# Performance work log

Hardware: AMD Instinct MI355X
Metric: run time of the kernel (lower is better)

## Reference

```python
import jax, jax.numpy as jnp
import numpy as np

NEG_SLOPE = 0.2
MASK_FILL = -1e9


def setup_inputs() -> dict:
    key = jax.random.key(0)
    k1, k2, k3, k4 = jax.random.split(key, 4)
    B, N, IN_DIM = 4, 2048, 256
    H, D = 8, 64  # n_heads, hidden_dim (out_dim)
    nodes = jax.random.normal(k1, (B, N, IN_DIM), dtype=jnp.float32)
    edges = jax.random.randint(k2, (B, N, N), 0, 2, dtype=jnp.int32)
    # Xavier-uniform-ish init for params
    pw_lim = float(np.sqrt(6.0 / (IN_DIM + H * D)))
    proj_weights = jax.random.uniform(k3, (IN_DIM, H * D), dtype=jnp.float32,
                                      minval=-pw_lim, maxval=pw_lim)
    aw_lim = float(np.sqrt(6.0 / (H + 2 * D)))
    attn_weights = jax.random.uniform(k4, (H, 2 * D), dtype=jnp.float32,
                                      minval=-aw_lim, maxval=aw_lim)
    return {"nodes": nodes, "edges": edges,
            "proj_weights": proj_weights, "attn_weights": attn_weights}


def reference(nodes, edges, proj_weights, attn_weights):
    B, N, _ = nodes.shape
    H, twoD = attn_weights.shape
    D = twoD // 2
    # Projection: [B,N,in] @ [in,H*D] -> [B,H,N,D]
    mapped = jnp.matmul(nodes, proj_weights).reshape(B, N, H, D).transpose(0, 2, 1, 3)
    # The left@diag(a)@right^T trick is exactly a_l.h_i + a_r.h_j:
    a_l = attn_weights[:, :D]   # [H,D]
    a_r = attn_weights[:, D:]   # [H,D]
    el = jnp.einsum('bhnd,hd->bhn', mapped, a_l)  # score contribution of source i
    er = jnp.einsum('bhnd,hd->bhn', mapped, a_r)  # score contribution of target j
    scores = jax.nn.leaky_relu(el[:, :, :, None] + er[:, :, None, :],
                               negative_slope=NEG_SLOPE)  # [B,H,N,N]
    scores = jnp.where(edges[:, None, :, :] == 0, MASK_FILL, scores)
    attn = jax.nn.softmax(scores, axis=-1)  # dropout p=0 -> identity
    out = jnp.einsum('bhij,bhjd->bhid', attn, mapped)  # [B,H,N,D]
    out = out.transpose(0, 2, 1, 3).reshape(B, N, H * D)  # is_concat=True
    return jax.nn.sigmoid(out)
```

## Files before the change

### kernel.cpp

```cpp
#include <hip/hip_runtime.h>
#include <hip/hip_fp16.h>
#include <math.h>

#define NEG 0.2f
#define LOG2E 1.4426950408889634f

typedef float f32x4 __attribute__((ext_vector_type(4)));
typedef _Float16 half8 __attribute__((ext_vector_type(8)));
typedef _Float16 h2v __attribute__((ext_vector_type(2)));

extern "C" __device__ _Float16 __ocml_exp2_f16(_Float16);

__device__ inline uint cvt2(float a, float b) {
  union {
    decltype(__builtin_amdgcn_cvt_pkrtz(0.f, 0.f)) v;
    uint u;
  } x;
  x.v = __builtin_amdgcn_cvt_pkrtz(a, b);
  return x.u;
}

__device__ inline h2v u2h(uint u) {
  union {
    uint u;
    h2v v;
  } x;
  x.u = u;
  return x.v;
}

__device__ inline uint h2u(h2v v) {
  union {
    uint u;
    h2v v;
  } x;
  x.v = v;
  return x.u;
}

__global__ __launch_bounds__(256) void prep_kernel(const float* __restrict__ W,
                                                   ushort* __restrict__ wf,
                                                   uint* __restrict__ ermx) {
  const int bx = blockIdx.x;
  const int t = threadIdx.x;
  if (bx == 32) {
    if (t < 32) ermx[t] = 0u;
    return;
  }
  const int h = bx >> 2, ct = bx & 3;
#pragma unroll
  for (int s = 0; s < 2; ++s) {
    int slot = t + s * 256;
    int l = slot & 63, kk = slot >> 6;
    int col = h * 64 + ct * 16 + (l & 15);
    int k0 = kk * 32 + (l >> 4) * 8;
    uint outv[4];
#pragma unroll
    for (int c = 0; c < 4; ++c) {
      float x0 = W[(size_t)(k0 + 2 * c) * 512 + col];
      float x1 = W[(size_t)(k0 + 2 * c + 1) * 512 + col];
      outv[c] = cvt2(x0, x1);
    }
    *(uint4*)&wf[(((size_t)((h * 4 + ct) * 8 + kk)) * 64 + l) * 8] = *(uint4*)outv;
  }
}

__global__ __launch_bounds__(256, 4) void pack_proj(
    const int* __restrict__ e, unsigned long long* __restrict__ epk64,
    const float* __restrict__ A, const ushort* __restrict__ wf,
    const float* __restrict__ aw, ushort* __restrict__ mt,
    float* __restrict__ el, float* __restrict__ er, uint* __restrict__ ermx) {
  __shared__ ushort ct_lds[64][72];
  const int bx = blockIdx.x;
  const int t = threadIdx.x;
  const int l = t & 63;
  if (bx % 5 != 4) {
    const int pack_id = (bx / 5) * 4 + (bx % 5);
    const int wid = pack_id * 4 + (t >> 6);
    const size_t base = (size_t)wid * 1024;
#pragma unroll
    for (int it = 0; it < 4; ++it) {
      const size_t off = base + it * 256;
      unsigned long long b0 = __ballot(e[off + l] != 0);
      unsigned long long b1 = __ballot(e[off + 64 + l] != 0);
      unsigned long long b2 = __ballot(e[off + 128 + l] != 0);
      unsigned long long b3 = __ballot(e[off + 192 + l] != 0);
      if (l == 0) {
        ulonglong2 p0, p1;
        p0.x = b0;
        p0.y = b1;
        p1.x = b2;
        p1.y = b3;
        *(ulonglong2*)&epk64[off >> 6] = p0;
        *(ulonglong2*)&epk64[(off >> 6) + 2] = p1;
      }
    }
    return;
  }
  const int pid = bx / 5;
  const int wq = t >> 6;
  const int i0 = (pid & 127) * 64;
  const int h = pid >> 7;
  const int b = i0 >> 11, n0 = i0 & 2047, bh = b * 8 + h;
  const int cl = l & 15, hi = l >> 4;
  const float* arow = A + (size_t)(i0 + wq * 16 + cl) * 256 + hi * 8;
  const int4* wfb = (const int4*)wf + (size_t)h * 32 * 64 + l;
  f32x4 acc[4];
#pragma unroll
  for (int ct = 0; ct < 4; ++ct) acc[ct] = (f32x4){0.f, 0.f, 0.f, 0.f};
#pragma unroll
  for (int kk = 0; kk < 8; ++kk) {
    float4 a0 = *(const float4*)(arow + kk * 32);
    float4 a1 = *(const float4*)(arow + kk * 32 + 4);
    union {
      uint u[4];
      half8 v;
    } af;
    af.u[0] = cvt2(a0.x, a0.y);
    af.u[1] = cvt2(a0.z, a0.w);
    af.u[2] = cvt2(a1.x, a1.y);
    af.u[3] = cvt2(a1.z, a1.w);
#pragma unroll
    for (int ct = 0; ct < 4; ++ct) {
      union {
        int4 i;
        half8 v;
      } bf;
      bf.i = wfb[((size_t)ct * 8 + kk) * 64];
      acc[ct] = __builtin_amdgcn_mfma_f32_16x16x32_f16(af.v, bf.v, acc[ct], 0, 0, 0);
    }
  }
  float alc[4], arc[4];
#pragma unroll
  for (int ct = 0; ct < 4; ++ct) {
    alc[ct] = aw[h * 128 + ct * 16 + cl];
    arc[ct] = aw[h * 128 + 64 + ct * 16 + cl];
  }
  float ermax_loc = -1e30f;
#pragma unroll
  for (int reg = 0; reg < 4; ++reg) {
    float pl = acc[0][reg] * alc[0] + acc[1][reg] * alc[1] + acc[2][reg] * alc[2] +
               acc[3][reg] * alc[3];
    float pr = acc[0][reg] * arc[0] + acc[1][reg] * arc[1] + acc[2][reg] * arc[2] +
               acc[3][reg] * arc[3];
#pragma unroll
    for (int s = 1; s < 16; s <<= 1) {
      pl += __shfl_xor(pl, s);
      pr += __shfl_xor(pr, s);
    }
    if (cl == 0) {
      int n = n0 + wq * 16 + hi * 4 + reg;
      el[(size_t)bh * 2048 + n] = pl;
      er[(size_t)bh * 2048 + n] = pr;
    }
    ermax_loc = fmaxf(ermax_loc, pr);
  }
  ermax_loc = fmaxf(ermax_loc, __shfl_xor(ermax_loc, 16));
  ermax_loc = fmaxf(ermax_loc, __shfl_xor(ermax_loc, 32));
  if (l == 0) {
    uint bits = __float_as_uint(ermax_loc);
    uint key = (bits & 0x80000000u) ? ~bits : (bits | 0x80000000u);
    atomicMax(&ermx[bh], key);
  }
#pragma unroll
  for (int ct = 0; ct < 4; ++ct) {
    ushort4 us;
    us.x = __half_as_ushort(__float2half(acc[ct][0]));
    us.y = __half_as_ushort(__float2half(acc[ct][1]));
    us.z = __half_as_ushort(__float2half(acc[ct][2]));
    us.w = __half_as_ushort(__float2half(acc[ct][3]));
    *(ushort4*)&ct_lds[ct * 16 + cl][wq * 16 + hi * 4] = us;
  }
  __syncthreads();
  {
    const int f = t >> 5, s = t & 31;
    const int g = f >> 2, nt = f & 3;
    const int r = nt * 16 + (s & 15);
    const int cm = g * 32 + (s >> 4) * 8;
    int4 v0 = *(const int4*)&ct_lds[r][cm];
    int4 v1 = *(const int4*)&ct_lds[r][cm + 16];
    const size_t base = ((size_t)bh * 32 + (n0 >> 6)) * 4096 + f * 512;
    *(int4*)&mt[base + s * 8] = v0;
    *(int4*)&mt[base + (s + 32) * 8] = v1;
  }
}

__global__ __launch_bounds__(512, 8) void gat_attn(const ushort* __restrict__ mt,
                                                   const uint* __restrict__ epk,
                                                   const float* __restrict__ el,
                                                   const float* __restrict__ er,
                                                   const uint* __restrict__ ermx,
                                                   float* __restrict__ out) {
  __shared__ __align__(16) char smem[36864];
  int4* vt4 = (int4*)smem;
  uint* ersh = (uint*)(smem + 32768);
  const int t = threadIdx.x;
  const int l = t & 63;
  const int hf = t >> 8;
  const int th = t & 255;
  const int wq = (t >> 6) & 3;
  const int r16 = l & 15, hi = l >> 4;
  const int sh8 = hi * 8;
  const int i0 = blockIdx.x * 64;
  const int h = blockIdx.y, b = blockIdx.z;
  const int bh = b * 8 + h;
  if (t < 256) {
    float4 e0 = *(const float4*)&er[(size_t)bh * 2048 + t * 8];
    float4 e1 = *(const float4*)&er[(size_t)bh * 2048 + t * 8 + 4];
    uint4 pk;
    pk.x = cvt2(e0.x, e0.y);
    pk.y = cvt2(e0.z, e0.w);
    pk.z = cvt2(e1.x, e1.y);
    pk.w = cvt2(e1.z, e1.w);
    *(uint4*)&ersh[t * 4] = pk;
  }
  const int irow = i0 + wq * 16 + r16;
  const float el_r = el[(size_t)bh * 2048 + irow];
  const uint ky = ermx[bh];
  const float emx = __uint_as_float((ky & 0x80000000u) ? (ky ^ 0x80000000u) : ~ky);
  const float s0 = el_r + emx;
  const float m_r = fmaxf(s0, NEG * s0);
  const float m2 = m_r * LOG2E;
  const float cAf = __builtin_fmaf(el_r, LOG2E, -m2);
  const float cBf = __builtin_fmaf(el_r, NEG * LOG2E, -m2);
  const h2v cA2 = {(_Float16)cAf, (_Float16)cAf};
  const h2v cB2 = {(_Float16)cBf, (_Float16)cBf};
  const h2v l2e2 = {(_Float16)LOG2E, (_Float16)LOG2E};
  const h2v nl2e2 = {(_Float16)(NEG * LOG2E), (_Float16)(NEG * LOG2E)};
  const uint* erow = epk + (size_t)(b * 2048 + irow) * 64;
  f32x4 acc[4];
  f32x4 accL = {0.f, 0.f, 0.f, 0.f};
#pragma unroll
  for (int nt = 0; nt < 4; ++nt) acc[nt] = (f32x4){0.f, 0.f, 0.f, 0.f};
  half8 ones;
#pragma unroll
  for (int c = 0; c < 8; ++c) ones[c] = (_Float16)1.f;

  const int jtg0 = hf * 16;
  const int4* srcbase = (const int4*)mt + ((size_t)bh * 32 + jtg0) * 512 + wq * 128 + l;
  unsigned long long ew = *(const unsigned long long*)(erow + jtg0 * 2);
  {
    int4 p0 = srcbase[0];
    int4 p1 = srcbase[64];
    int4* d = vt4 + hf * 512 + wq * 128 + l;
    d[0] = p0;
    d[64] = p1;
  }
  __syncthreads();
  int cur = 0;
  for (int jt = 0; jt < 16; ++jt) {
    int4 nx0, nx1;
    unsigned long long ewn;
    if (jt < 15) {
      const int4* s = srcbase + (size_t)(jt + 1) * 512;
      nx0 = s[0];
      nx1 = s[64];
      ewn = *(const unsigned long long*)(erow + (jtg0 + jt + 1) * 2);
    }
    const uint wsh0 = ((uint)ew) >> sh8;
    const uint wsh1 = ((uint)(ew >> 32)) >> sh8;
    const int j0 = (jtg0 + jt) * 64;
    half8 af[2];
#pragma unroll
    for (int g = 0; g < 2; ++g) {
      uint4 uv = *(const uint4*)&ersh[(j0 >> 1) + g * 16 + hi * 4];
      uint uvw[4] = {uv.x, uv.y, uv.z, uv.w};
      const uint wg = g ? wsh1 : wsh0;
      union {
        uint u[4];
        half8 v8;
      } fr;
#pragma unroll
      for (int q = 0; q < 4; ++q) {
        h2v u2 = u2h(uvw[q]);
#if __has_builtin(__builtin_elementwise_fma)
        h2v a2 = __builtin_elementwise_fma(u2, l2e2, cA2);
        h2v b2 = __builtin_elementwise_fma(u2, nl2e2, cB2);
#else
        h2v a2 = u2 * l2e2 + cA2;
        h2v b2 = u2 * nl2e2 + cB2;
#endif
        h2v t2 = __builtin_elementwise_max(a2, b2);
        h2v p2;
        p2[0] = __ocml_exp2_f16(t2[0]);
        p2[1] = __ocml_exp2_f16(t2[1]);
        uint pu = h2u(p2);
        uint mlo = (uint)(((int)(wg << (31 - 2 * q))) >> 31);
        uint mhi = (uint)(((int)(wg << (30 - 2 * q))) >> 31);
        uint mask2 = (mlo & 0x0000FFFFu) | (mhi & 0xFFFF0000u);
        fr.u[q] = pu & mask2;
      }
      af[g] = fr.v8;
    }
    const half8* fb = (const half8*)(vt4 + cur * 1024 + hf * 512);
    __builtin_amdgcn_s_setprio(1);
#pragma unroll
    for (int g = 0; g < 2; ++g) {
      accL = __builtin_amdgcn_mfma_f32_16x16x32_f16(af[g], ones, accL, 0, 0, 0);
#pragma unroll
      for (int nt = 0; nt < 4; ++nt) {
        half8 bfr = fb[(g * 4 + nt) * 64 + l];
        acc[nt] = __builtin_amdgcn_mfma_f32_16x16x32_f16(af[g], bfr, acc[nt], 0, 0, 0);
      }
    }
    __builtin_amdgcn_s_setprio(0);
    if (jt < 15) {
      int4* d = vt4 + (cur ^ 1) * 1024 + hf * 512 + wq * 128 + l;
      d[0] = nx0;
      d[64] = nx1;
      ew = ewn;
    }
    __syncthreads();
    cur ^= 1;
  }
  float* red = (float*)smem;
  if (hf == 1) {
    float* dst = red + th * 21;
#pragma unroll
    for (int nt = 0; nt < 4; ++nt)
#pragma unroll
      for (int k = 0; k < 4; ++k) dst[nt * 4 + k] = acc[nt][k];
#pragma unroll
    for (int k = 0; k < 4; ++k) dst[16 + k] = accL[k];
  }
  __syncthreads();
  if (hf == 0) {
    const float* src = red + th * 21;
#pragma unroll
    for (int reg = 0; reg < 4; ++reg) {
      float Lrow = accL[reg] + src[16 + reg];
      float invL = 1.f / Lrow;
      int orow = i0 + wq * 16 + hi * 4 + reg;
#pragma unroll
      for (int nt = 0; nt < 4; ++nt) {
        float o = (acc[nt][reg] + src[nt * 4 + reg]) * invL;
        float sig = 1.f / (1.f + __expf(-o));
        out[(size_t)(b * 2048 + orow) * 512 + h * 64 + nt * 16 + r16] = sig;
      }
    }
  }
}

extern "C" void kernel_launch(void* const* d_in, const int* in_sizes, int n_in,
                              void* d_out, int out_size, void* d_ws, size_t ws_size,
                              hipStream_t stream) {
  const float* nodes = (const float*)d_in[0];
  const int* edges = (const int*)d_in[1];
  const float* pw = (const float*)d_in[2];
  const float* aw = (const float*)d_in[3];
  float* out = (float*)d_out;

  ushort* mt = (ushort*)d_ws;
  float* el = (float*)((char*)d_ws + 8388608);
  float* er = (float*)((char*)d_ws + 8650752);
  uint* ermx = (uint*)((char*)d_ws + 8912896);
  uint* epk = (uint*)((char*)d_ws + 8913024);
  ushort* wf = (ushort*)((char*)d_ws + 11010176);

  prep_kernel<<<33, 256, 0, stream>>>(pw, wf, ermx);
  pack_proj<<<5120, 256, 0, stream>>>(edges, (unsigned long long*)epk, nodes, wf, aw,
                                      mt, el, er, ermx);
  gat_attn<<<dim3(32, 8, 4), 512, 0, stream>>>(mt, epk, el, er, ermx, out);
}
```

Measured before the change: 91.33 us.

## Factor softmax exponent into precomputed exp terms and restructure edge bitmask packing

Uses exp(a+b) = exp(a)*exp(b) to precompute per-column exp2 factors for both leaky-relu branches in shared memory and per-row scale factors. The per-element exp2 in the inner loop becomes two fp16 multiplies and a max. Edge packing now loads int4 vectors with an interleaved bit layout, and half of the packing is moved into the prep kernel so it runs ahead of the projection. The risks are fp16 overflow or underflow of the exp factors, since er is unbounded, and more complex bit extraction.

```diff
diff --git a/kernel.cpp b/kernel.cpp
--- a/kernel.cpp
+++ b/kernel.cpp
@@ -8,8 +8,13 @@
 typedef float f32x4 __attribute__((ext_vector_type(4)));
 typedef _Float16 half8 __attribute__((ext_vector_type(8)));
 typedef _Float16 h2v __attribute__((ext_vector_type(2)));
-
-extern "C" __device__ _Float16 __ocml_exp2_f16(_Float16);
+typedef short s16x2 __attribute__((ext_vector_type(2)));
+
+#if __has_builtin(__builtin_amdgcn_exp2f)
+#define EXP2F(x) __builtin_amdgcn_exp2f(x)
+#else
+#define EXP2F(x) exp2f(x)
+#endif
 
 __device__ inline uint cvt2(float a, float b) {
   union {
@@ -38,34 +43,67 @@
   return x.u;
 }
 
-__global__ __launch_bounds__(256) void prep_kernel(const float* __restrict__ W,
-                                                   ushort* __restrict__ wf,
-                                                   uint* __restrict__ ermx) {
+__device__ inline uint sgn16(uint t) {
+  union {
+    uint u;
+    s16x2 v;
+  } x;
+  x.u = t;
+  x.v = x.v >> 15;
+  return x.u;
+}
+
+__global__ __launch_bounds__(256, 4) void prep_pack(
+    const float* __restrict__ W, ushort* __restrict__ wf, uint* __restrict__ ermx,
+    const int* __restrict__ e, unsigned long long* __restrict__ epk64) {
   const int bx = blockIdx.x;
   const int t = threadIdx.x;
-  if (bx == 32) {
-    if (t < 32) ermx[t] = 0u;
+  const int l = t & 63;
+  if (bx < 33) {
+    if (bx == 32) {
+      if (t < 32) ermx[t] = 0u;
+      return;
+    }
+    const int h = bx >> 2, ct = bx & 3;
+#pragma unroll
+    for (int s = 0; s < 2; ++s) {
+      int slot = t + s * 256;
+      int ll = slot & 63, kk = slot >> 6;
+      int col = h * 64 + ct * 16 + (ll & 15);
+      int k0 = kk * 32 + (ll >> 4) * 8;
+      uint outv[4];
+#pragma unroll
+      for (int c = 0; c < 4; ++c) {
+        float x0 = W[(size_t)(k0 + 2 * c) * 512 + col];
+        float x1 = W[(size_t)(k0 + 2 * c + 1) * 512 + col];
+        outv[c] = cvt2(x0, x1);
+      }
+      *(uint4*)&wf[(((size_t)((h * 4 + ct) * 8 + kk)) * 64 + ll) * 8] = *(uint4*)outv;
+    }
     return;
   }
-  const int h = bx >> 2, ct = bx & 3;
-#pragma unroll
-  for (int s = 0; s < 2; ++s) {
-    int slot = t + s * 256;
-    int l = slot & 63, kk = slot >> 6;
-    int col = h * 64 + ct * 16 + (l & 15);
-    int k0 = kk * 32 + (l >> 4) * 8;
-    uint outv[4];
-#pragma unroll
-    for (int c = 0; c < 4; ++c) {
-      float x0 = W[(size_t)(k0 + 2 * c) * 512 + col];
-      float x1 = W[(size_t)(k0 + 2 * c + 1) * 512 + col];
-      outv[c] = cvt2(x0, x1);
-    }
-    *(uint4*)&wf[(((size_t)((h * 4 + ct) * 8 + kk)) * 64 + l) * 8] = *(uint4*)outv;
-  }
-}
-
-__global__ __launch_bounds__(256, 4) void pack_proj(
+  const size_t g0 = (size_t)(bx - 33) * 16 + (t >> 6) * 4;
+#pragma unroll
+  for (int it = 0; it < 4; ++it) {
+    const size_t gi = g0 + it;
+    int4 v = *(const int4*)(e + gi * 256 + l * 4);
+    unsigned long long b0 = __ballot(v.x != 0);
+    unsigned long long b1 = __ballot(v.y != 0);
+    unsigned long long b2 = __ballot(v.z != 0);
+    unsigned long long b3 = __ballot(v.w != 0);
+    if (l == 0) {
+      ulonglong2 q0, q1;
+      q0.x = b0;
+      q0.y = b1;
+      q1.x = b2;
+      q1.y = b3;
+      *(ulonglong2*)&epk64[gi * 4] = q0;
+      *(ulonglong2*)&epk64[gi * 4 + 2] = q1;
+    }
+  }
+}
+
+__global__ __launch_bounds__(256, 4) void pack2_proj(
     const int* __restrict__ e, unsigned long long* __restrict__ epk64,
     const float* __restrict__ A, const ushort* __restrict__ wf,
     const float* __restrict__ aw, ushort* __restrict__ mt,
@@ -74,30 +112,30 @@
   const int bx = blockIdx.x;
   const int t = threadIdx.x;
   const int l = t & 63;
-  if (bx % 5 != 4) {
-    const int pack_id = (bx / 5) * 4 + (bx % 5);
-    const int wid = pack_id * 4 + (t >> 6);
-    const size_t base = (size_t)wid * 1024;
+  if (bx % 3 != 2) {
+    const int pb = (bx / 3) * 2 + (bx % 3);
+    const size_t g0 = 32768 + (size_t)pb * 16 + (t >> 6) * 4;
 #pragma unroll
     for (int it = 0; it < 4; ++it) {
-      const size_t off = base + it * 256;
-      unsigned long long b0 = __ballot(e[off + l] != 0);
-      unsigned long long b1 = __ballot(e[off + 64 + l] != 0);
-      unsigned long long b2 = __ballot(e[off + 128 + l] != 0);
-      unsigned long long b3 = __ballot(e[off + 192 + l] != 0);
+      const size_t gi = g0 + it;
+      int4 v = *(const int4*)(e + gi * 256 + l * 4);
+      unsigned long long b0 = __ballot(v.x != 0);
+      unsigned long long b1 = __ballot(v.y != 0);
+      unsigned long long b2 = __ballot(v.z != 0);
+      unsigned long long b3 = __ballot(v.w != 0);
       if (l == 0) {
-        ulonglong2 p0, p1;
-        p0.x = b0;
-        p0.y = b1;
-        p1.x = b2;
-        p1.y = b3;
-        *(ulonglong2*)&epk64[off >> 6] = p0;
-        *(ulonglong2*)&epk64[(off >> 6) + 2] = p1;
+        ulonglong2 q0, q1;
+        q0.x = b0;
+        q0.y = b1;
+        q1.x = b2;
+        q1.y = b3;
+        *(ulonglong2*)&epk64[gi * 4] = q0;
+        *(ulonglong2*)&epk64[gi * 4 + 2] = q1;
       }
     }
     return;
   }
-  const int pid = bx / 5;
+  const int pid = bx / 3;
   const int wq = t >> 6;
   const int i0 = (pid & 127) * 64;
   const int h = pid >> 7;
@@ -185,49 +223,45 @@
   }
 }
 
-__global__ __launch_bounds__(512, 8) void gat_attn(const ushort* __restrict__ mt,
-                                                   const uint* __restrict__ epk,
-                                                   const float* __restrict__ el,
-                                                   const float* __restrict__ er,
-                                                   const uint* __restrict__ ermx,
-                                                   float* __restrict__ out) {
-  __shared__ __align__(16) char smem[36864];
+__global__ __launch_bounds__(512, 8) void gat_attn(
+    const ushort* __restrict__ mt, const unsigned long long* __restrict__ epk64,
+    const float* __restrict__ el, const float* __restrict__ er,
+    const uint* __restrict__ ermx, float* __restrict__ out) {
+  __shared__ __align__(16) char smem[40960];
   int4* vt4 = (int4*)smem;
-  uint* ersh = (uint*)(smem + 32768);
+  uint* ysh = (uint*)(smem + 32768);
+  uint* vsh = (uint*)(smem + 36864);
   const int t = threadIdx.x;
   const int l = t & 63;
   const int hf = t >> 8;
   const int th = t & 255;
   const int wq = (t >> 6) & 3;
   const int r16 = l & 15, hi = l >> 4;
-  const int sh8 = hi * 8;
   const int i0 = blockIdx.x * 64;
   const int h = blockIdx.y, b = blockIdx.z;
   const int bh = b * 8 + h;
-  if (t < 256) {
-    float4 e0 = *(const float4*)&er[(size_t)bh * 2048 + t * 8];
-    float4 e1 = *(const float4*)&er[(size_t)bh * 2048 + t * 8 + 4];
-    uint4 pk;
-    pk.x = cvt2(e0.x, e0.y);
-    pk.y = cvt2(e0.z, e0.w);
-    pk.z = cvt2(e1.x, e1.y);
-    pk.w = cvt2(e1.z, e1.w);
-    *(uint4*)&ersh[t * 4] = pk;
+  {
+    float4 e0 = *(const float4*)&er[(size_t)bh * 2048 + t * 4];
+    uint2 yp, vp;
+    yp.x = cvt2(EXP2F(e0.x * LOG2E), EXP2F(e0.y * LOG2E));
+    yp.y = cvt2(EXP2F(e0.z * LOG2E), EXP2F(e0.w * LOG2E));
+    vp.x = cvt2(EXP2F(e0.x * (NEG * LOG2E)), EXP2F(e0.y * (NEG * LOG2E)));
+    vp.y = cvt2(EXP2F(e0.z * (NEG * LOG2E)), EXP2F(e0.w * (NEG * LOG2E)));
+    *(uint2*)&ysh[t * 2] = yp;
+    *(uint2*)&vsh[t * 2] = vp;
   }
   const int irow = i0 + wq * 16 + r16;
   const float el_r = el[(size_t)bh * 2048 + irow];
   const uint ky = ermx[bh];
   const float emx = __uint_as_float((ky & 0x80000000u) ? (ky ^ 0x80000000u) : ~ky);
   const float s0 = el_r + emx;
-  const float m_r = fmaxf(s0, NEG * s0);
-  const float m2 = m_r * LOG2E;
-  const float cAf = __builtin_fmaf(el_r, LOG2E, -m2);
-  const float cBf = __builtin_fmaf(el_r, NEG * LOG2E, -m2);
-  const h2v cA2 = {(_Float16)cAf, (_Float16)cAf};
-  const h2v cB2 = {(_Float16)cBf, (_Float16)cBf};
-  const h2v l2e2 = {(_Float16)LOG2E, (_Float16)LOG2E};
-  const h2v nl2e2 = {(_Float16)(NEG * LOG2E), (_Float16)(NEG * LOG2E)};
-  const uint* erow = epk + (size_t)(b * 2048 + irow) * 64;
+  const float m2 = fmaxf(s0, NEG * s0) * LOG2E;
+  const float Xf = EXP2F(__builtin_fmaf(el_r, LOG2E, -m2));
+  const float Uf = EXP2F(__builtin_fmaf(el_r, NEG * LOG2E, -m2));
+  const h2v X2 = u2h(cvt2(Xf, Xf));
+  const h2v U2 = u2h(cvt2(Uf, Uf));
+  const unsigned long long* prow =
+      epk64 + ((size_t)(b * 2048 + irow) * 8 + hf * 4) * 4;
   f32x4 acc[4];
   f32x4 accL = {0.f, 0.f, 0.f, 0.f};
 #pragma unroll
@@ -236,9 +270,7 @@
 #pragma unroll
   for (int c = 0; c < 8; ++c) ones[c] = (_Float16)1.f;
 
-  const int jtg0 = hf * 16;
-  const int4* srcbase = (const int4*)mt + ((size_t)bh * 32 + jtg0) * 512 + wq * 128 + l;
-  unsigned long long ew = *(const unsigned long long*)(erow + jtg0 * 2);
+  const int4* srcbase = (const int4*)mt + ((size_t)bh * 32 + hf * 16) * 512 + wq * 128 + l;
   {
     int4 p0 = srcbase[0];
     int4 p1 = srcbase[64];
@@ -248,70 +280,66 @@
   }
   __syncthreads();
   int cur = 0;
-  for (int jt = 0; jt < 16; ++jt) {
-    int4 nx0, nx1;
-    unsigned long long ewn;
-    if (jt < 15) {
-      const int4* s = srcbase + (size_t)(jt + 1) * 512;
-      nx0 = s[0];
-      nx1 = s[64];
-      ewn = *(const unsigned long long*)(erow + (jtg0 + jt + 1) * 2);
-    }
-    const uint wsh0 = ((uint)ew) >> sh8;
-    const uint wsh1 = ((uint)(ew >> 32)) >> sh8;
-    const int j0 = (jtg0 + jt) * 64;
-    half8 af[2];
-#pragma unroll
-    for (int g = 0; g < 2; ++g) {
-      uint4 uv = *(const uint4*)&ersh[(j0 >> 1) + g * 16 + hi * 4];
-      uint uvw[4] = {uv.x, uv.y, uv.z, uv.w};
-      const uint wg = g ? wsh1 : wsh0;
-      union {
-        uint u[4];
-        half8 v8;
-      } fr;
-#pragma unroll
-      for (int q = 0; q < 4; ++q) {
-        h2v u2 = u2h(uvw[q]);
-#if __has_builtin(__builtin_elementwise_fma)
-        h2v a2 = __builtin_elementwise_fma(u2, l2e2, cA2);
-        h2v b2 = __builtin_elementwise_fma(u2, nl2e2, cB2);
-#else
-        h2v a2 = u2 * l2e2 + cA2;
-        h2v b2 = u2 * nl2e2 + cB2;
-#endif
-        h2v t2 = __builtin_elementwise_max(a2, b2);
-        h2v p2;
-        p2[0] = __ocml_exp2_f16(t2[0]);
-        p2[1] = __ocml_exp2_f16(t2[1]);
-        uint pu = h2u(p2);
-        uint mlo = (uint)(((int)(wg << (31 - 2 * q))) >> 31);
-        uint mhi = (uint)(((int)(wg << (30 - 2 * q))) >> 31);
-        uint mask2 = (mlo & 0x0000FFFFu) | (mhi & 0xFFFF0000u);
-        fr.u[q] = pu & mask2;
-      }
-      af[g] = fr.v8;
-    }
-    const half8* fb = (const half8*)(vt4 + cur * 1024 + hf * 512);
-    __builtin_amdgcn_s_setprio(1);
-#pragma unroll
-    for (int g = 0; g < 2; ++g) {
-      accL = __builtin_amdgcn_mfma_f32_16x16x32_f16(af[g], ones, accL, 0, 0, 0);
-#pragma unroll
-      for (int nt = 0; nt < 4; ++nt) {
-        half8 bfr = fb[(g * 4 + nt) * 64 + l];
-        acc[nt] = __builtin_amdgcn_mfma_f32_16x16x32_f16(af[g], bfr, acc[nt], 0, 0, 0);
-      }
-    }
-    __builtin_amdgcn_s_setprio(0);
-    if (jt < 15) {
-      int4* d = vt4 + (cur ^ 1) * 1024 + hf * 512 + wq * 128 + l;
-      d[0] = nx0;
-      d[64] = nx1;
-      ew = ewn;
-    }
-    __syncthreads();
-    cur ^= 1;
+  int jt = 0;
+  for (int gq = 0; gq < 4; ++gq) {
+    const ulonglong2 pA = *(const ulonglong2*)(prow + gq * 4);
+    const ulonglong2 pB = *(const ulonglong2*)(prow + gq * 4 + 2);
+#pragma unroll
+    for (int q4 = 0; q4 < 4; ++q4, ++jt) {
+      int4 nx0, nx1;
+      if (jt < 15) {
+        const int4* s = srcbase + (size_t)(jt + 1) * 512;
+        nx0 = s[0];
+        nx1 = s[64];
+      }
+      const int Bb = q4 * 16 + hi * 2;
+      half8 af[2];
+#pragma unroll
+      for (int g = 0; g < 2; ++g) {
+        const uint idx = (hf * 16 + jt) * 32 + g * 16 + hi * 4;
+        uint4 y4 = *(const uint4*)&ysh[idx];
+        uint4 v4 = *(const uint4*)&vsh[idx];
+        const int sh = Bb + g * 8;
+        uint w0 = (uint)(pA.x >> sh), w1 = (uint)(pA.y >> sh);
+        uint w2 = (uint)(pB.x >> sh), w3 = (uint)(pB.y >> sh);
+        uint tk0 = ((w0 << 15) & 0x8000u) | (w1 << 31);
+        uint tk1 = ((w2 << 15) & 0x8000u) | (w3 << 31);
+        uint tk2 = ((w0 << 14) & 0x8000u) | ((w1 << 30) & 0x80000000u);
+        uint tk3 = ((w2 << 14) & 0x8000u) | ((w3 << 30) & 0x80000000u);
+        uint yq[4] = {y4.x, y4.y, y4.z, y4.w};
+        uint vq[4] = {v4.x, v4.y, v4.z, v4.w};
+        uint tq[4] = {tk0, tk1, tk2, tk3};
+        union {
+          uint u[4];
+          half8 v8;
+        } fr;
+#pragma unroll
+        for (int q = 0; q < 4; ++q) {
+          h2v P2 = __builtin_elementwise_max(X2 * u2h(yq[q]), U2 * u2h(vq[q]));
+          fr.u[q] = h2u(P2) & sgn16(tq[q]);
+        }
+        af[g] = fr.v8;
+      }
+      const half8* fb = (const half8*)(vt4 + cur * 1024 + hf * 512);
+      __builtin_amdgcn_s_setprio(1);
+#pragma unroll
+      for (int g = 0; g < 2; ++g) {
+        accL = __builtin_amdgcn_mfma_f32_16x16x32_f16(af[g], ones, accL, 0, 0, 0);
+#pragma unroll
+        for (int nt = 0; nt < 4; ++nt) {
+          half8 bfr = fb[(g * 4 + nt) * 64 + l];
+          acc[nt] = __builtin_amdgcn_mfma_f32_16x16x32_f16(af[g], bfr, acc[nt], 0, 0, 0);
+        }
+      }
+      __builtin_amdgcn_s_setprio(0);
+      if (jt < 15) {
+        int4* d = vt4 + (cur ^ 1) * 1024 + hf * 512 + wq * 128 + l;
+        d[0] = nx0;
+        d[64] = nx1;
+      }
+      __syncthreads();
+      cur ^= 1;
+    }
   }
   float* red = (float*)smem;
   if (hf == 1) {
@@ -354,11 +382,10 @@
   float* el = (float*)((char*)d_ws + 8388608);
   float* er = (float*)((char*)d_ws + 8650752);
   uint* ermx = (uint*)((char*)d_ws + 8912896);
-  uint* epk = (uint*)((char*)d_ws + 8913024);
+  unsigned long long* epk = (unsigned long long*)((char*)d_ws + 8913024);
   ushort* wf = (ushort*)((char*)d_ws + 11010176);
 
-  prep_kernel<<<33, 256, 0, stream>>>(pw, wf, ermx);
-  pack_proj<<<5120, 256, 0, stream>>>(edges, (unsigned long long*)epk, nodes, wf, aw,
-                                      mt, el, er, ermx);
+  prep_pack<<<2081, 256, 0, stream>>>(pw, wf, ermx, edges, epk);
+  pack2_proj<<<3072, 256, 0, stream>>>(edges, epk, nodes, wf, aw, mt, el, er, ermx);
   gat_attn<<<dim3(32, 8, 4), 512, 0, stream>>>(mt, epk, el, er, ermx, out);
 }
```

Result: slower. 160.3 us (+75.5%).

## Move half of edge-mask packing into the weight-prep kernel

Applied to the files above, without the earlier changes.

The edge bitmask packing is split across two launches. The first half of the edge rows is now packed alongside the weight conversion in the first kernel, and the second kernel interleaves the remaining packing with the projection blocks at a 2:1 ratio instead of 4:1. The aim is to fill the nearly idle prep launch with bandwidth-bound work and shorten the projection kernel. In exchange the first kernel becomes much larger and has to finish before projection starts.

```diff
diff --git a/kernel.cpp b/kernel.cpp
--- a/kernel.cpp
+++ b/kernel.cpp
@@ -38,34 +38,57 @@
   return x.u;
 }
 
-__global__ __launch_bounds__(256) void prep_kernel(const float* __restrict__ W,
-                                                   ushort* __restrict__ wf,
-                                                   uint* __restrict__ ermx) {
+__global__ __launch_bounds__(256, 4) void prep_pack(
+    const float* __restrict__ W, ushort* __restrict__ wf, uint* __restrict__ ermx,
+    const int* __restrict__ e, unsigned long long* __restrict__ epk64) {
   const int bx = blockIdx.x;
   const int t = threadIdx.x;
-  if (bx == 32) {
-    if (t < 32) ermx[t] = 0u;
+  const int l = t & 63;
+  if (bx < 33) {
+    if (bx == 32) {
+      if (t < 32) ermx[t] = 0u;
+      return;
+    }
+    const int h = bx >> 2, ct = bx & 3;
+#pragma unroll
+    for (int s = 0; s < 2; ++s) {
+      int slot = t + s * 256;
+      int ll = slot & 63, kk = slot >> 6;
+      int col = h * 64 + ct * 16 + (ll & 15);
+      int k0 = kk * 32 + (ll >> 4) * 8;
+      uint outv[4];
+#pragma unroll
+      for (int c = 0; c < 4; ++c) {
+        float x0 = W[(size_t)(k0 + 2 * c) * 512 + col];
+        float x1 = W[(size_t)(k0 + 2 * c + 1) * 512 + col];
+        outv[c] = cvt2(x0, x1);
+      }
+      *(uint4*)&wf[(((size_t)((h * 4 + ct) * 8 + kk)) * 64 + ll) * 8] = *(uint4*)outv;
+    }
     return;
   }
-  const int h = bx >> 2, ct = bx & 3;
-#pragma unroll
-  for (int s = 0; s < 2; ++s) {
-    int slot = t + s * 256;
-    int l = slot & 63, kk = slot >> 6;
-    int col = h * 64 + ct * 16 + (l & 15);
-    int k0 = kk * 32 + (l >> 4) * 8;
-    uint outv[4];
-#pragma unroll
-    for (int c = 0; c < 4; ++c) {
-      float x0 = W[(size_t)(k0 + 2 * c) * 512 + col];
-      float x1 = W[(size_t)(k0 + 2 * c + 1) * 512 + col];
-      outv[c] = cvt2(x0, x1);
-    }
-    *(uint4*)&wf[(((size_t)((h * 4 + ct) * 8 + kk)) * 64 + l) * 8] = *(uint4*)outv;
-  }
-}
-
-__global__ __launch_bounds__(256, 4) void pack_proj(
+  const size_t g0 = (size_t)(bx - 33) * 16 + (t >> 6) * 4;
+#pragma unroll
+  for (int it = 0; it < 4; ++it) {
+    const size_t gi = g0 + it;
+    const int* ep = e + gi * 256;
+    unsigned long long b0 = __ballot(ep[l] != 0);
+    unsigned long long b1 = __ballot(ep[64 + l] != 0);
+    unsigned long long b2 = __ballot(ep[128 + l] != 0);
+    unsigned long long b3 = __ballot(ep[192 + l] != 0);
+    if (l == 0) {
+      ulonglong2 q0, q1;
+      q0.x = b0;
+      q0.y = b1;
+      q1.x = b2;
+      q1.y = b3;
+      *(ulonglong2*)&epk64[gi * 4] = q0;
+      *(ulonglong2*)&epk64[gi * 4 + 2] = q1;
+    }
+  }
+}
+
+__global__ __launch_bounds__(256, 4) void pack2_proj(
     const int* __restrict__ e, unsigned long long* __restrict__ epk64,
     const float* __restrict__ A, const ushort* __restrict__ wf,
     const float* __restrict__ aw, ushort* __restrict__ mt,
@@ -74,30 +97,30 @@
   const int bx = blockIdx.x;
   const int t = threadIdx.x;
   const int l = t & 63;
-  if (bx % 5 != 4) {
-    const int pack_id = (bx / 5) * 4 + (bx % 5);
-    const int wid = pack_id * 4 + (t >> 6);
-    const size_t base = (size_t)wid * 1024;
+  if (bx % 3 != 2) {
+    const int pb = (bx / 3) * 2 + (bx % 3);
+    const size_t g0 = 32768 + (size_t)pb * 16 + (t >> 6) * 4;
 #pragma unroll
     for (int it = 0; it < 4; ++it) {
-      const size_t off = base + it * 256;
-      unsigned long long b0 = __ballot(e[off + l] != 0);
-      unsigned long long b1 = __ballot(e[off + 64 + l] != 0);
-      unsigned long long b2 = __ballot(e[off + 128 + l] != 0);
-      unsigned long long b3 = __ballot(e[off + 192 + l] != 0);
+      const size_t gi = g0 + it;
+      const int* ep = e + gi * 256;
+      unsigned long long b0 = __ballot(ep[l] != 0);
+      unsigned long long b1 = __ballot(ep[64 + l] != 0);
+      unsigned long long b2 = __ballot(ep[128 + l] != 0);
+      unsigned long long b3 = __ballot(ep[192 + l] != 0);
       if (l == 0) {
-        ulonglong2 p0, p1;
-        p0.x = b0;
-        p0.y = b1;
-        p1.x = b2;
-        p1.y = b3;
-        *(ulonglong2*)&epk64[off >> 6] = p0;
-        *(ulonglong2*)&epk64[(off >> 6) + 2] = p1;
+        ulonglong2 q0, q1;
+        q0.x = b0;
+        q0.y = b1;
+        q1.x = b2;
+        q1.y = b3;
+        *(ulonglong2*)&epk64[gi * 4] = q0;
+        *(ulonglong2*)&epk64[gi * 4 + 2] = q1;
       }
     }
     return;
   }
-  const int pid = bx / 5;
+  const int pid = bx / 3;
   const int wq = t >> 6;
   const int i0 = (pid & 127) * 64;
   const int h = pid >> 7;
@@ -354,11 +377,10 @@
   float* el = (float*)((char*)d_ws + 8388608);
   float* er = (float*)((char*)d_ws + 8650752);
   uint* ermx = (uint*)((char*)d_ws + 8912896);
-  uint* epk = (uint*)((char*)d_ws + 8913024);
+  unsigned long long* epk = (unsigned long long*)((char*)d_ws + 8913024);
   ushort* wf = (ushort*)((char*)d_ws + 11010176);
 
-  prep_kernel<<<33, 256, 0, stream>>>(pw, wf, ermx);
-  pack_proj<<<5120, 256, 0, stream>>>(edges, (unsigned long long*)epk, nodes, wf, aw,
-                                      mt, el, er, ermx);
-  gat_attn<<<dim3(32, 8, 4), 512, 0, stream>>>(mt, epk, el, er, ermx, out);
-}
+  prep_pack<<<2081, 256, 0, stream>>>(pw, wf, ermx, edges, epk);
+  pack2_proj<<<3072, 256, 0, stream>>>(edges, epk, nodes, wf, aw, mt, el, er, ermx);
+  gat_attn<<<dim3(32, 8, 4), 512, 0, stream>>>(mt, (const uint*)epk, el, er, ermx, out);
+}
```

After: 92.86 us. No clear change (+1.7%).
